# Kernel tuning notes

Hardware: AMD Instinct MI355X
Metric: run time of the kernel (lower is better)

Reference implementation:

```python
import jax, jax.numpy as jnp
import numpy as np

N_NODES = 100000
N_EDGES = 1600000
N_GRAPHS = 128


def setup_inputs() -> dict:
    key = jax.random.key(0)
    ks = jax.random.split(key, 8)
    x = jax.random.normal(ks[0], (N_NODES, 384), dtype=jnp.float32)
    edge_index = jax.random.randint(ks[1], (2, N_EDGES), 0, N_NODES, dtype=jnp.int64)
    batch = jnp.sort(jax.random.randint(ks[2], (N_NODES,), 0, N_GRAPHS, dtype=jnp.int64))
    W1 = jax.random.normal(ks[3], (384, 128), dtype=jnp.float32) * (1.0 / np.sqrt(384))
    b1 = jnp.zeros((128,), dtype=jnp.float32)
    W2 = jax.random.normal(ks[4], (128, 64), dtype=jnp.float32) * (1.0 / np.sqrt(128))
    b2 = jnp.zeros((64,), dtype=jnp.float32)
    Wlin = jax.random.normal(ks[5], (64, 2), dtype=jnp.float32) * (1.0 / np.sqrt(64))
    blin = jnp.zeros((2,), dtype=jnp.float32)
    return {"x": x, "edge_index": edge_index, "batch": batch,
            "W1": W1, "b1": b1, "W2": W2, "b2": b2, "Wlin": Wlin, "blin": blin}


def gcn_conv(x, src, dst, W, b, n_nodes):
    # PyG GCNConv: self-loops + symmetric normalization D^{-1/2} A_hat D^{-1/2},
    # linear transform first (out_dim < in_dim -> cheaper messages).
    h = x @ W  # [N, out]
    deg = jax.ops.segment_sum(jnp.ones_like(dst, dtype=h.dtype), dst,
                              num_segments=n_nodes) + 1.0  # self-loop weight
    dis = jax.lax.rsqrt(deg)  # deg >= 1 always (self-loop)
    norm = dis[src] * dis[dst]  # per-edge normalization [E]
    msg = h[src] * norm[:, None]  # gather + scale [E, out]
    agg = jax.ops.segment_sum(msg, dst, num_segments=n_nodes)
    agg = agg + h * (dis * dis)[:, None]  # self-loop contribution
    return agg + b


def reference(x, edge_index, batch, W1, b1, W2, b2, Wlin, blin):
    src, dst = edge_index[0], edge_index[1]
    n_nodes = x.shape[0]
    h = jax.nn.relu(gcn_conv(x, src, dst, W1, b1, n_nodes))
    h = jax.nn.relu(gcn_conv(h, src, dst, W2, b2, n_nodes))
    # global_mean_pool over graph ids
    sums = jax.ops.segment_sum(h, batch, num_segments=N_GRAPHS)
    cnts = jax.ops.segment_sum(jnp.ones((n_nodes,), dtype=h.dtype), batch,
                               num_segments=N_GRAPHS)
    pooled = sums / jnp.maximum(cnts, 1.0)[:, None]  # [G, 64]
    # dropout is identity in eval mode
    return pooled @ Wlin + blin  # [G, 2]
```

## Files before the change

kernel.cpp:

```cpp
#include <hip/hip_runtime.h>


#define NN 100000
#define NG 128
#define BNODES 256
#define NBUK ((NN + BNODES - 1) / BNODES)
#define BCAP 6144

typedef __attribute__((ext_vector_type(8))) short short8;
typedef __attribute__((ext_vector_type(8))) unsigned short u16x8;
typedef __attribute__((ext_vector_type(4))) float f32x4;

__device__ __forceinline__ unsigned short f2bf(float f) {
    union { float f; unsigned u; } v; v.f = f;
    unsigned r = v.u + 0x7fffu + ((v.u >> 16) & 1u);
    return (unsigned short)(r >> 16);
}
__device__ __forceinline__ float bf2f(unsigned short h) {
    union { unsigned u; float f; } v; v.u = ((unsigned)h) << 16;
    return v.f;
}

__device__ __forceinline__ void gload_lds16(const void* g, void* l) {
    __builtin_amdgcn_global_load_lds(
        (const __attribute__((address_space(1))) void*)g,
        (__attribute__((address_space(3))) void*)l, 16, 0, 0);
}

__global__ __launch_bounds__(256) void init_kernel(int* __restrict__ bcnt,
                                                   float* __restrict__ pooled,
                                                   float* __restrict__ cnt) {
    const int i = blockIdx.x * 256 + threadIdx.x;
    if (i < NBUK) bcnt[i] = 0;
    if (i < NG * 64) pooled[i] = 0.f;
    if (i < NG) cnt[i] = 0.f;
}

__global__ __launch_bounds__(256) void bucket_scatter(const int* __restrict__ src,
                                                      const int* __restrict__ dst,
                                                      int* __restrict__ bcnt,
                                                      int2* __restrict__ pairs, int E) {
    __shared__ int hist[NBUK];
    __shared__ int lbase[NBUK];
    __shared__ int lfill[NBUK];
    const int t = threadIdx.x;
    const int chunk = (E + gridDim.x - 1) / gridDim.x;
    const int lo = blockIdx.x * chunk;
    const int hi = min(E, lo + chunk);
    for (int b = t; b < NBUK; b += 256) { hist[b] = 0; lfill[b] = 0; }
    __syncthreads();
    for (int i = lo + t; i < hi; i += 256)
        atomicAdd(&hist[dst[i] >> 8], 1);
    __syncthreads();
    for (int b = t; b < NBUK; b += 256)
        lbase[b] = hist[b] ? atomicAdd(&bcnt[b], hist[b]) : 0;
    __syncthreads();
    for (int i = lo + t; i < hi; i += 256) {
        const int s = src[i], d = dst[i];
        const int b = d >> 8;
        const int off = atomicAdd(&lfill[b], 1);
        pairs[(size_t)b * BCAP + lbase[b] + off] = make_int2(s, d);
    }
}

__global__ __launch_bounds__(512) void bucket_scan(const int* __restrict__ bcnt,
                                                   int* __restrict__ bbase,
                                                   int* __restrict__ rowptr,
                                                   int N, int E) {
    __shared__ int sm[512];
    const int t = threadIdx.x;
    sm[t] = (t < NBUK) ? bcnt[t] : 0;
    __syncthreads();
    for (int d = 1; d < 512; d <<= 1) {
        int a = (t >= d) ? sm[t - d] : 0;
        __syncthreads();
        sm[t] += a;
        __syncthreads();
    }
    if (t <= NBUK) bbase[t] = (t == 0) ? 0 : sm[t - 1];
    if (t == 0) rowptr[N] = E;
}

__global__ __launch_bounds__(256) void bucket_build(const int2* __restrict__ pairs,
                                                    const int* __restrict__ bcnt,
                                                    const int* __restrict__ bbase,
                                                    int* __restrict__ rowptr,
                                                    float* __restrict__ dis,
                                                    int* __restrict__ col, int N) {
    __shared__ int cnt[BNODES];
    __shared__ int sm[BNODES];
    __shared__ int pref[BNODES];
    __shared__ int fillc[BNODES];
    const int b = blockIdx.x;
    const int t = threadIdx.x;
    const int nbase = b * BNODES;
    const int ecnt = bcnt[b];
    const int2* ep = pairs + (size_t)b * BCAP;
    const int gbase = bbase[b];

    cnt[t] = 0;
    fillc[t] = 0;
    __syncthreads();
    for (int i = t; i < ecnt; i += 256)
        atomicAdd(&cnt[ep[i].y & (BNODES - 1)], 1);
    __syncthreads();
    sm[t] = cnt[t];
    __syncthreads();
    for (int d = 1; d < 256; d <<= 1) {
        int a = (t >= d) ? sm[t - d] : 0;
        __syncthreads();
        sm[t] += a;
        __syncthreads();
    }
    pref[t] = sm[t] - cnt[t];
    const int node = nbase + t;
    if (node < N) {
        rowptr[node] = gbase + pref[t];
        dis[node] = rsqrtf((float)cnt[t] + 1.0f);
    }
    __syncthreads();
    for (int i = t; i < ecnt; i += 256) {
        const int2 e = ep[i];
        const int d = e.y & (BNODES - 1);
        const int pos = gbase + pref[d] + atomicAdd(&fillc[d], 1);
        col[pos] = e.x;
    }
}

__global__ __launch_bounds__(256) void pack_w(const float* __restrict__ W,
                                              unsigned short* __restrict__ packH,
                                              unsigned short* __restrict__ packL,
                                              int K, int BN) {
    const int idx = blockIdx.x * blockDim.x + threadIdx.x;
    if (idx >= K * BN) return;
    const int e = idx & 7;
    const int l = (idx >> 3) & 63;
    const int rest = idx >> 9;
    const int NF = BN >> 4;
    const int nf = rest % NF;
    const int ks = rest / NF;
    const int n = nf * 16 + (l & 15);
    const int k = ks * 32 + ((l >> 4) & 3) * 8 + e;
    const float v = W[(size_t)k * BN + n];
    const unsigned short h = f2bf(v);
    packH[idx] = h;
    packL[idx] = f2bf(v - bf2f(h));
}

template <int BN, int K>
__global__ __launch_bounds__(256) void gemm_mfma(const float* __restrict__ A,
                                                 const unsigned short* __restrict__ WpH,
                                                 const unsigned short* __restrict__ WpL,
                                                 const float* __restrict__ scale,
                                                 unsigned short* __restrict__ Out,
                                                 int N) {
    constexpr int BM = 64;
    constexpr int NK = K / 32;
    constexpr int WROWS = (BN == 128) ? 2 : 4;
    constexpr int WCOLS = (BN == 128) ? 2 : 1;
    constexpr int WTM = BM / WROWS;
    constexpr int MF = WTM / 16;
    constexpr int NFW = (BN / WCOLS) / 16;
    constexpr int NFB = BN / 16;

    __shared__ float AsF[4][4][16][32];

    const int t = threadIdx.x;
    const int wid = t >> 6, lane = t & 63;
    const int wr = wid / WCOLS, wc = wid % WCOLS;
    const int r0 = blockIdx.x * BM;

    const int dmarow0 = min(r0 + wid * 16 + (lane >> 3), NN - 1);
    const int dmarow1 = min(r0 + wid * 16 + 8 + (lane >> 3), NN - 1);
    const float* dmap0 = A + (size_t)dmarow0 * K + (lane & 7) * 4;
    const float* dmap1 = A + (size_t)dmarow1 * K + (lane & 7) * 4;

    auto stageA = [&](int buf, int ks) {
        gload_lds16(dmap0 + ks * 32, &AsF[buf][wid][0][0]);
        gload_lds16(dmap1 + ks * 32, &AsF[buf][wid][8][0]);
    };
    auto loadB = [&](int ks, short8* bH, short8* bL) {
#pragma unroll
        for (int n = 0; n < NFW; ++n) {
            const int nfg = wc * NFW + n;
            const int base = ((ks * NFB + nfg) * 64 + lane) * 8;
            bH[n] = *(const short8*)&WpH[base];
            bL[n] = *(const short8*)&WpL[base];
        }
    };

    f32x4 acc[MF][NFW];
#pragma unroll
    for (int m = 0; m < MF; ++m)
#pragma unroll
        for (int n = 0; n < NFW; ++n) acc[m][n] = (f32x4){0.f, 0.f, 0.f, 0.f};

    short8 bHc[NFW], bLc[NFW];
    loadB(0, bHc, bLc);
    stageA(0, 0);
    if (NK > 1) stageA(1, 1);
    if (NK > 2) stageA(2, 2);

#pragma unroll
    for (int ks = 0; ks < NK; ++ks) {
        if (ks == NK - 1) {
            asm volatile("s_waitcnt vmcnt(0)" ::: "memory");
        } else {
            asm volatile("s_waitcnt vmcnt(4)" ::: "memory");
        }
        __builtin_amdgcn_s_barrier();
        short8 bHn[NFW], bLn[NFW];
        if (ks + 1 < NK) loadB(ks + 1, bHn, bLn);
        if (ks + 3 < NK) stageA((ks + 3) & 3, ks + 3);
        const int cur = ks & 3;
#pragma unroll
        for (int m = 0; m < MF; ++m) {
            const int mf = wr * MF + m;
            const float* fp = &AsF[cur][mf][lane & 15][(lane >> 4) * 8];
            const f32x4 f0 = *(const f32x4*)fp;
            const f32x4 f1 = *(const f32x4*)(fp + 4);
            short8 aH;
            aH[0] = (short)f2bf(f0[0]);
            aH[1] = (short)f2bf(f0[1]);
            aH[2] = (short)f2bf(f0[2]);
            aH[3] = (short)f2bf(f0[3]);
            aH[4] = (short)f2bf(f1[0]);
            aH[5] = (short)f2bf(f1[1]);
            aH[6] = (short)f2bf(f1[2]);
            aH[7] = (short)f2bf(f1[3]);
#pragma unroll
            for (int n = 0; n < NFW; ++n) {
                acc[m][n] = __builtin_amdgcn_mfma_f32_16x16x32_bf16(aH, bHc[n], acc[m][n], 0, 0, 0);
                acc[m][n] = __builtin_amdgcn_mfma_f32_16x16x32_bf16(aH, bLc[n], acc[m][n], 0, 0, 0);
            }
        }
        if (ks + 1 < NK) {
#pragma unroll
            for (int n = 0; n < NFW; ++n) {
                bHc[n] = bHn[n];
                bLc[n] = bLn[n];
            }
        }
    }

#pragma unroll
    for (int m = 0; m < MF; ++m) {
        const int row0 = r0 + wr * WTM + m * 16 + ((lane >> 4) << 2);
        float sc[4];
#pragma unroll
        for (int r = 0; r < 4; ++r) sc[r] = (row0 + r < N) ? scale[row0 + r] : 0.f;
#pragma unroll
        for (int n = 0; n < NFW; ++n) {
            const int cn = wc * (NFW * 16) + n * 16 + (lane & 15);
#pragma unroll
            for (int r = 0; r < 4; ++r) {
                if (row0 + r < N)
                    Out[(size_t)(row0 + r) * BN + cn] = f2bf(acc[m][n][r] * sc[r]);
            }
        }
    }
}

template <int BN, int K>
__global__ __launch_bounds__(256) void gemm_mfma_b(const unsigned short* __restrict__ A,
                                                   const unsigned short* __restrict__ WpH,
                                                   const unsigned short* __restrict__ WpL,
                                                   const float* __restrict__ scale,
                                                   unsigned short* __restrict__ Out,
                                                   int N) {
    constexpr int BM = 64;
    constexpr int NK = K / 32;
    constexpr int WROWS = 4;
    constexpr int WTM = BM / WROWS;
    constexpr int NFW = BN / 16;
    constexpr int NFB = BN / 16;

    __shared__ unsigned short AsB[4][4][16][32];

    const int t = threadIdx.x;
    const int wid = t >> 6, lane = t & 63;
    const int wr = wid;
    const int r0 = blockIdx.x * BM;

    const int dmarow = min(r0 + wid * 16 + (lane >> 2), NN - 1);
    const unsigned short* dmap = A + (size_t)dmarow * K + (lane & 3) * 8;

    auto stageA = [&](int buf, int ks) {
        gload_lds16(dmap + ks * 32, &AsB[buf][wid][0][0]);
    };
    auto loadB = [&](int ks, short8* bH, short8* bL) {
#pragma unroll
        for (int n = 0; n < NFW; ++n) {
            const int base = ((ks * NFB + n) * 64 + lane) * 8;
            bH[n] = *(const short8*)&WpH[base];
            bL[n] = *(const short8*)&WpL[base];
        }
    };

    f32x4 acc[NFW];
#pragma unroll
    for (int n = 0; n < NFW; ++n) acc[n] = (f32x4){0.f, 0.f, 0.f, 0.f};

    short8 bHc[NFW], bLc[NFW];
    loadB(0, bHc, bLc);
    stageA(0, 0);
    if (NK > 1) stageA(1, 1);
    if (NK > 2) stageA(2, 2);

#pragma unroll
    for (int ks = 0; ks < NK; ++ks) {
        if (ks == NK - 1) {
            asm volatile("s_waitcnt vmcnt(0)" ::: "memory");
        } else if (ks == 0) {
            asm volatile("s_waitcnt vmcnt(2)" ::: "memory");
        } else {
            asm volatile("s_waitcnt vmcnt(4)" ::: "memory");
        }
        __builtin_amdgcn_s_barrier();
        short8 bHn[NFW], bLn[NFW];
        if (ks + 1 < NK) loadB(ks + 1, bHn, bLn);
        if (ks + 3 < NK) stageA((ks + 3) & 3, ks + 3);
        const int cur = ks & 3;
        const short8 aH = *(const short8*)&AsB[cur][wr][lane & 15][(lane >> 4) * 8];
#pragma unroll
        for (int n = 0; n < NFW; ++n) {
            acc[n] = __builtin_amdgcn_mfma_f32_16x16x32_bf16(aH, bHc[n], acc[n], 0, 0, 0);
            acc[n] = __builtin_amdgcn_mfma_f32_16x16x32_bf16(aH, bLc[n], acc[n], 0, 0, 0);
        }
        if (ks + 1 < NK) {
#pragma unroll
            for (int n = 0; n < NFW; ++n) {
                bHc[n] = bHn[n];
                bLc[n] = bLn[n];
            }
        }
    }

    const int row0 = r0 + wr * WTM + ((lane >> 4) << 2);
    float sc[4];
#pragma unroll
    for (int r = 0; r < 4; ++r) sc[r] = (row0 + r < N) ? scale[row0 + r] : 0.f;
#pragma unroll
    for (int n = 0; n < NFW; ++n) {
        const int cn = n * 16 + (lane & 15);
#pragma unroll
        for (int r = 0; r < 4; ++r) {
            if (row0 + r < N)
                Out[(size_t)(row0 + r) * BN + cn] = f2bf(acc[n][r] * sc[r]);
        }
    }
}

template <int COLS, bool OB16>
__global__ __launch_bounds__(256) void agg_gather(const int* __restrict__ rowptr,
                                                  const int* __restrict__ col,
                                                  const float* __restrict__ dis,
                                                  const unsigned short* __restrict__ Hs,
                                                  const float* __restrict__ bias,
                                                  void* __restrict__ OutV, int N) {
    constexpr int NPW = (COLS == 128) ? 1 : 2;
    constexpr int LPN = 64 / NPW;
    constexpr int LPR = COLS / 8;
    constexpr int NSG = LPN / LPR;
    const int gw = (int)((blockIdx.x * blockDim.x + threadIdx.x) >> 6);
    const int lane = threadIdx.x & 63;
    const int sub = lane / LPN;
    const int nl = lane % LPN;
    const int esub = nl / LPR;
    const int sl = nl % LPR;
    const int node = gw * NPW + sub;
    const int lgbase = sub * LPN;

    float acc[8];
#pragma unroll
    for (int k = 0; k < 8; ++k) acc[k] = 0.f;

    int base = 0, len = 0;
    const int nodec = (node < N) ? node : 0;
    if (node < N) {
        base = rowptr[node];
        len = rowptr[node + 1] - base;
    }

    for (int j0 = 0; j0 < len; j0 += LPN) {
        const int remain = min(LPN, len - j0);
        const int sidx = (nl < remain) ? col[base + j0 + nl] : nodec;
        const int qtr = (remain + NSG - 1) / NSG;
        const int off = esub * qtr;
        int u = 0;
        for (; u + 8 <= qtr; u += 8) {
            u16x8 hv[8];
            float wv[8];
#pragma unroll
            for (int b = 0; b < 8; ++b) {
                const int idx = off + u + b;
                const int s = __shfl(sidx, lgbase + idx);
                wv[b] = (idx < remain) ? 1.f : 0.f;
                hv[b] = *(const u16x8*)(Hs + (size_t)s * COLS + sl * 8);
            }
#pragma unroll
            for (int b = 0; b < 8; ++b)
#pragma unroll
                for (int k = 0; k < 8; ++k)
                    acc[k] = fmaf(bf2f(hv[b][k]), wv[b], acc[k]);
        }
        for (; u + 4 <= qtr; u += 4) {
            u16x8 hv[4];
            float wv[4];
#pragma unroll
            for (int b = 0; b < 4; ++b) {
                const int idx = off + u + b;
                const int s = __shfl(sidx, lgbase + idx);
                wv[b] = (idx < remain) ? 1.f : 0.f;
                hv[b] = *(const u16x8*)(Hs + (size_t)s * COLS + sl * 8);
            }
#pragma unroll
            for (int b = 0; b < 4; ++b)
#pragma unroll
                for (int k = 0; k < 8; ++k)
                    acc[k] = fmaf(bf2f(hv[b][k]), wv[b], acc[k]);
        }
        for (; u < qtr; ++u) {
            const int idx = off + u;
            const int s = __shfl(sidx, lgbase + idx);
            const float w = (idx < remain) ? 1.f : 0.f;
            const u16x8 hv = *(const u16x8*)(Hs + (size_t)s * COLS + sl * 8);
#pragma unroll
            for (int k = 0; k < 8; ++k)
                acc[k] = fmaf(bf2f(hv[k]), w, acc[k]);
        }
    }

#pragma unroll
    for (int k = 0; k < 8; ++k) {
        acc[k] += __shfl_xor(acc[k], LPR);
        acc[k] += __shfl_xor(acc[k], 2 * LPR);
    }

    if (node < N && esub == 0) {
        const float dd = dis[node];
        const u16x8 hsb = *(const u16x8*)(Hs + (size_t)node * COLS + sl * 8);
        float o[8];
#pragma unroll
        for (int k = 0; k < 8; ++k)
            o[k] = fmaxf(fmaf(acc[k] + bf2f(hsb[k]), dd, bias[sl * 8 + k]), 0.f);
        if (OB16) {
            u16x8 ob;
#pragma unroll
            for (int k = 0; k < 8; ++k) ob[k] = f2bf(o[k]);
            *(u16x8*)((unsigned short*)OutV + (size_t)node * COLS + sl * 8) = ob;
        } else {
            float* Out = (float*)OutV;
            f32x4 o0, o1;
#pragma unroll
            for (int k = 0; k < 4; ++k) {
                o0[k] = o[k];
                o1[k] = o[k + 4];
            }
            *(f32x4*)(Out + (size_t)node * COLS + sl * 8) = o0;
            *(f32x4*)(Out + (size_t)node * COLS + sl * 8 + 4) = o1;
        }
    }
}

__global__ __launch_bounds__(256) void pool_kernel(const float* __restrict__ H,
                                                   const int* __restrict__ batch,
                                                   float* __restrict__ pooled,
                                                   float* __restrict__ cnt, int N) {
    const int c = threadIdx.x & 63;
    const int w = threadIdx.x >> 6;
    const int row0 = blockIdx.x * 128 + w * 32;
    if (row0 >= N) return;
    const int nr = min(32, N - row0);

    float v[32];
    int b[32];
#pragma unroll
    for (int i = 0; i < 32; ++i) {
        const int r = row0 + i;
        if (i < nr) {
            v[i] = H[(size_t)r * 64 + c];
            b[i] = batch[r];
        } else {
            v[i] = 0.f;
            b[i] = -1;
        }
    }
    int cur = b[0];
    float sum = 0.f, csum = 0.f;
#pragma unroll
    for (int i = 0; i < 32; ++i) {
        if (i < nr) {
            if (b[i] != cur) {
                atomicAdd(&pooled[cur * 64 + c], sum);
                if (c == 0) atomicAdd(&cnt[cur], csum);
                cur = b[i];
                sum = 0.f;
                csum = 0.f;
            }
            sum += v[i];
            csum += 1.f;
        }
    }
    atomicAdd(&pooled[cur * 64 + c], sum);
    if (c == 0) atomicAdd(&cnt[cur], csum);
}

__global__ __launch_bounds__(256) void final_kernel(const float* __restrict__ pooled,
                                                    const float* __restrict__ cnt,
                                                    const float* __restrict__ Wlin,
                                                    const float* __restrict__ blin,
                                                    float* __restrict__ out) {
    const int t = threadIdx.x;
    const int g = t >> 1, o = t & 1;
    const float inv = 1.0f / fmaxf(cnt[g], 1.0f);
    float s = 0.f;
#pragma unroll
    for (int j = 0; j < 64; ++j) s = fmaf(pooled[g * 64 + j], Wlin[j * 2 + o], s);
    out[t] = s * inv + blin[o];
}

extern "C" void kernel_launch(void* const* d_in, const int* in_sizes, int n_in,
                              void* d_out, int out_size, void* d_ws, size_t ws_size,
                              hipStream_t stream) {
    const float* x     = (const float*)d_in[0];
    const int*   edge  = (const int*)d_in[1];
    const int*   batch = (const int*)d_in[2];
    const float* W1    = (const float*)d_in[3];
    const float* b1    = (const float*)d_in[4];
    const float* W2    = (const float*)d_in[5];
    const float* b2    = (const float*)d_in[6];
    const float* Wlin  = (const float*)d_in[7];
    const float* blin  = (const float*)d_in[8];
    float* out = (float*)d_out;

    const int N = NN;
    const int E = in_sizes[1] / 2;
    const int* src = edge;
    const int* dst = edge + E;

    char* ws = (char*)d_ws;
    size_t off = 0;
    auto alloc = [&](size_t bytes) -> void* {
        void* p = ws + off;
        off += (bytes + 511) & ~(size_t)511;
        return p;
    };
    float* dis    = (float*)alloc((size_t)N * 4);
    int*   rowptr = (int*)alloc((size_t)(N + 1) * 4);
    int*   bcnt   = (int*)alloc((size_t)NBUK * 4);
    int*   bbase  = (int*)alloc((size_t)(NBUK + 1) * 4);
    int*   col    = (int*)alloc((size_t)E * 4);
    int2*  pairs  = (int2*)alloc((size_t)NBUK * BCAP * 8);
    unsigned short* w1h = (unsigned short*)alloc((size_t)384 * 128 * 2);
    unsigned short* w1l = (unsigned short*)alloc((size_t)384 * 128 * 2);
    unsigned short* w2h = (unsigned short*)alloc((size_t)128 * 64 * 2);
    unsigned short* w2l = (unsigned short*)alloc((size_t)128 * 64 * 2);
    unsigned short* h1bf   = (unsigned short*)alloc((size_t)N * 128 * 2);
    unsigned short* agg1bf = (unsigned short*)alloc((size_t)N * 128 * 2);
    float* pooled = (float*)alloc((size_t)NG * 64 * 4);
    float* cnt    = (float*)alloc((size_t)NG * 4);
    unsigned short* h2bf = h1bf;
    float* agg2 = (float*)agg1bf;

    init_kernel<<<(NG * 64 + 255) / 256, 256, 0, stream>>>(bcnt, pooled, cnt);

    pack_w<<<(384 * 128 + 255) / 256, 256, 0, stream>>>(W1, w1h, w1l, 384, 128);
    pack_w<<<(128 * 64 + 255) / 256, 256, 0, stream>>>(W2, w2h, w2l, 128, 64);

    bucket_scatter<<<512, 256, 0, stream>>>(src, dst, bcnt, pairs, E);
    bucket_scan<<<1, 512, 0, stream>>>(bcnt, bbase, rowptr, N, E);
    bucket_build<<<NBUK, 256, 0, stream>>>(pairs, bcnt, bbase, rowptr, dis, col, N);

    const int gblocks = (N + 63) / 64;
    gemm_mfma<128, 384><<<gblocks, 256, 0, stream>>>(x, w1h, w1l, dis, h1bf, N);
    agg_gather<128, true><<<(N + 3) / 4, 256, 0, stream>>>(rowptr, col, dis, h1bf, b1,
                                                           (void*)agg1bf, N);

    gemm_mfma_b<64, 128><<<gblocks, 256, 0, stream>>>(agg1bf, w2h, w2l, dis, h2bf, N);
    agg_gather<64, false><<<(N + 7) / 8, 256, 0, stream>>>(rowptr, col, dis, h2bf, b2,
                                                           (void*)agg2, N);

    pool_kernel<<<(N + 127) / 128, 256, 0, stream>>>(agg2, batch, pooled, cnt, N);
    final_kernel<<<1, 256, 0, stream>>>(pooled, cnt, Wlin, blin, out);
}
```

Measured before the change: 236.2 us.

## Fuse second aggregation with mean pooling and pack bucket edge pairs

The second-layer gather aggregation now feeds global mean pooling directly. Each block stages its 8 node rows in shared memory and reduces runs of the same graph before issuing atomics, so the fp32 N×64 intermediate and the separate pool kernel go away. Bucket pairs are also packed into one 32-bit word (low 8 dst bits plus 24-bit src), which halves the scatter and build traffic. The packing assumes node ids fit in 24 bits, and pooling now does more per-block atomics with a block-wide sync.

```diff
diff --git a/kernel.cpp b/kernel.cpp
--- a/kernel.cpp
+++ b/kernel.cpp
@@ -39,7 +39,7 @@
 __global__ __launch_bounds__(256) void bucket_scatter(const int* __restrict__ src,
                                                       const int* __restrict__ dst,
                                                       int* __restrict__ bcnt,
-                                                      int2* __restrict__ pairs, int E) {
+                                                      int* __restrict__ pairs, int E) {
     __shared__ int hist[NBUK];
     __shared__ int lbase[NBUK];
     __shared__ int lfill[NBUK];
@@ -59,7 +59,7 @@
         const int s = src[i], d = dst[i];
         const int b = d >> 8;
         const int off = atomicAdd(&lfill[b], 1);
-        pairs[(size_t)b * BCAP + lbase[b] + off] = make_int2(s, d);
+        pairs[(size_t)b * BCAP + lbase[b] + off] = ((d & 255) << 24) | s;
     }
 }
 
@@ -81,7 +81,7 @@
     if (t == 0) rowptr[N] = E;
 }
 
-__global__ __launch_bounds__(256) void bucket_build(const int2* __restrict__ pairs,
+__global__ __launch_bounds__(256) void bucket_build(const int* __restrict__ pairs,
                                                     const int* __restrict__ bcnt,
                                                     const int* __restrict__ bbase,
                                                     int* __restrict__ rowptr,
@@ -95,14 +95,14 @@
     const int t = threadIdx.x;
     const int nbase = b * BNODES;
     const int ecnt = bcnt[b];
-    const int2* ep = pairs + (size_t)b * BCAP;
+    const int* ep = pairs + (size_t)b * BCAP;
     const int gbase = bbase[b];
 
     cnt[t] = 0;
     fillc[t] = 0;
     __syncthreads();
     for (int i = t; i < ecnt; i += 256)
-        atomicAdd(&cnt[ep[i].y & (BNODES - 1)], 1);
+        atomicAdd(&cnt[((unsigned)ep[i]) >> 24], 1);
     __syncthreads();
     sm[t] = cnt[t];
     __syncthreads();
@@ -120,10 +120,10 @@
     }
     __syncthreads();
     for (int i = t; i < ecnt; i += 256) {
-        const int2 e = ep[i];
-        const int d = e.y & (BNODES - 1);
+        const int p = ep[i];
+        const int d = ((unsigned)p) >> 24;
         const int pos = gbase + pref[d] + atomicAdd(&fillc[d], 1);
-        col[pos] = e.x;
+        col[pos] = p & 0xFFFFFF;
     }
 }
 
@@ -351,25 +351,24 @@
     }
 }
 
-template <int COLS, bool OB16>
-__global__ __launch_bounds__(256) void agg_gather(const int* __restrict__ rowptr,
-                                                  const int* __restrict__ col,
-                                                  const float* __restrict__ dis,
-                                                  const unsigned short* __restrict__ Hs,
-                                                  const float* __restrict__ bias,
-                                                  void* __restrict__ OutV, int N) {
-    constexpr int NPW = (COLS == 128) ? 1 : 2;
-    constexpr int LPN = 64 / NPW;
+__global__ __launch_bounds__(256) void agg_gather128(const int* __restrict__ rowptr,
+                                                     const int* __restrict__ col,
+                                                     const float* __restrict__ dis,
+                                                     const unsigned short* __restrict__ Hs,
+                                                     const float* __restrict__ bias,
+                                                     unsigned short* __restrict__ Out,
+                                                     int N) {
+    constexpr int COLS = 128;
+    constexpr int LPN = 64;
     constexpr int LPR = COLS / 8;
-    constexpr int NSG = LPN / LPR;
+    constexpr int NSG = 4;
     const int gw = (int)((blockIdx.x * blockDim.x + threadIdx.x) >> 6);
     const int lane = threadIdx.x & 63;
-    const int sub = lane / LPN;
-    const int nl = lane % LPN;
+    const int nl = lane;
     const int esub = nl / LPR;
     const int sl = nl % LPR;
-    const int node = gw * NPW + sub;
-    const int lgbase = sub * LPN;
+    const int node = gw;
+    const int lgbase = 0;
 
     float acc[8];
 #pragma unroll
@@ -440,70 +439,145 @@
     if (node < N && esub == 0) {
         const float dd = dis[node];
         const u16x8 hsb = *(const u16x8*)(Hs + (size_t)node * COLS + sl * 8);
-        float o[8];
+        u16x8 ob;
 #pragma unroll
         for (int k = 0; k < 8; ++k)
-            o[k] = fmaxf(fmaf(acc[k] + bf2f(hsb[k]), dd, bias[sl * 8 + k]), 0.f);
-        if (OB16) {
-            u16x8 ob;
-#pragma unroll
-            for (int k = 0; k < 8; ++k) ob[k] = f2bf(o[k]);
-            *(u16x8*)((unsigned short*)OutV + (size_t)node * COLS + sl * 8) = ob;
-        } else {
-            float* Out = (float*)OutV;
-            f32x4 o0, o1;
-#pragma unroll
-            for (int k = 0; k < 4; ++k) {
-                o0[k] = o[k];
-                o1[k] = o[k + 4];
-            }
-            *(f32x4*)(Out + (size_t)node * COLS + sl * 8) = o0;
-            *(f32x4*)(Out + (size_t)node * COLS + sl * 8 + 4) = o1;
-        }
-    }
-}
-
-__global__ __launch_bounds__(256) void pool_kernel(const float* __restrict__ H,
-                                                   const int* __restrict__ batch,
-                                                   float* __restrict__ pooled,
-                                                   float* __restrict__ cnt, int N) {
-    const int c = threadIdx.x & 63;
-    const int w = threadIdx.x >> 6;
-    const int row0 = blockIdx.x * 128 + w * 32;
-    if (row0 >= N) return;
-    const int nr = min(32, N - row0);
-
-    float v[32];
-    int b[32];
-#pragma unroll
-    for (int i = 0; i < 32; ++i) {
-        const int r = row0 + i;
-        if (i < nr) {
-            v[i] = H[(size_t)r * 64 + c];
-            b[i] = batch[r];
-        } else {
-            v[i] = 0.f;
-            b[i] = -1;
-        }
-    }
-    int cur = b[0];
-    float sum = 0.f, csum = 0.f;
-#pragma unroll
-    for (int i = 0; i < 32; ++i) {
-        if (i < nr) {
-            if (b[i] != cur) {
-                atomicAdd(&pooled[cur * 64 + c], sum);
-                if (c == 0) atomicAdd(&cnt[cur], csum);
-                cur = b[i];
-                sum = 0.f;
-                csum = 0.f;
-            }
-            sum += v[i];
-            csum += 1.f;
-        }
-    }
-    atomicAdd(&pooled[cur * 64 + c], sum);
-    if (c == 0) atomicAdd(&cnt[cur], csum);
+            ob[k] = f2bf(fmaxf(fmaf(acc[k] + bf2f(hsb[k]), dd, bias[sl * 8 + k]), 0.f));
+        *(u16x8*)(Out + (size_t)node * COLS + sl * 8) = ob;
+    }
+}
+
+__global__ __launch_bounds__(256) void agg_pool(const int* __restrict__ rowptr,
+                                                const int* __restrict__ col,
+                                                const float* __restrict__ dis,
+                                                const unsigned short* __restrict__ Hs,
+                                                const float* __restrict__ bias,
+                                                const int* __restrict__ batch,
+                                                float* __restrict__ pooled,
+                                                float* __restrict__ cnt, int N) {
+    constexpr int COLS = 64;
+    constexpr int NPW = 2;
+    constexpr int LPN = 32;
+    constexpr int LPR = COLS / 8;
+    constexpr int NSG = 4;
+
+    __shared__ float pbuf[8][64];
+    __shared__ int pg[8];
+
+    const int t = threadIdx.x;
+    const int wid = t >> 6;
+    const int gw = (int)blockIdx.x * 4 + wid;
+    const int lane = t & 63;
+    const int sub = lane / LPN;
+    const int nl = lane % LPN;
+    const int esub = nl / LPR;
+    const int sl = nl % LPR;
+    const int node = gw * NPW + sub;
+    const int slot = wid * 2 + sub;
+    const int lgbase = sub * LPN;
+
+    float acc[8];
+#pragma unroll
+    for (int k = 0; k < 8; ++k) acc[k] = 0.f;
+
+    int base = 0, len = 0;
+    const int nodec = (node < N) ? node : 0;
+    if (node < N) {
+        base = rowptr[node];
+        len = rowptr[node + 1] - base;
+    }
+
+    for (int j0 = 0; j0 < len; j0 += LPN) {
+        const int remain = min(LPN, len - j0);
+        const int sidx = (nl < remain) ? col[base + j0 + nl] : nodec;
+        const int qtr = (remain + NSG - 1) / NSG;
+        const int off = esub * qtr;
+        int u = 0;
+        for (; u + 8 <= qtr; u += 8) {
+            u16x8 hv[8];
+            float wv[8];
+#pragma unroll
+            for (int b = 0; b < 8; ++b) {
+                const int idx = off + u + b;
+                const int s = __shfl(sidx, lgbase + idx);
+                wv[b] = (idx < remain) ? 1.f : 0.f;
+                hv[b] = *(const u16x8*)(Hs + (size_t)s * COLS + sl * 8);
+            }
+#pragma unroll
+            for (int b = 0; b < 8; ++b)
+#pragma unroll
+                for (int k = 0; k < 8; ++k)
+                    acc[k] = fmaf(bf2f(hv[b][k]), wv[b], acc[k]);
+        }
+        for (; u + 4 <= qtr; u += 4) {
+            u16x8 hv[4];
+            float wv[4];
+#pragma unroll
+            for (int b = 0; b < 4; ++b) {
+                const int idx = off + u + b;
+                const int s = __shfl(sidx, lgbase + idx);
+                wv[b] = (idx < remain) ? 1.f : 0.f;
+                hv[b] = *(const u16x8*)(Hs + (size_t)s * COLS + sl * 8);
+            }
+#pragma unroll
+            for (int b = 0; b < 4; ++b)
+#pragma unroll
+                for (int k = 0; k < 8; ++k)
+                    acc[k] = fmaf(bf2f(hv[b][k]), wv[b], acc[k]);
+        }
+        for (; u < qtr; ++u) {
+            const int idx = off + u;
+            const int s = __shfl(sidx, lgbase + idx);
+            const float w = (idx < remain) ? 1.f : 0.f;
+            const u16x8 hv = *(const u16x8*)(Hs + (size_t)s * COLS + sl * 8);
+#pragma unroll
+            for (int k = 0; k < 8; ++k)
+                acc[k] = fmaf(bf2f(hv[k]), w, acc[k]);
+        }
+    }
+
+#pragma unroll
+    for (int k = 0; k < 8; ++k) {
+        acc[k] += __shfl_xor(acc[k], LPR);
+        acc[k] += __shfl_xor(acc[k], 2 * LPR);
+    }
+
+    if (esub == 0) {
+        const float dd = dis[nodec];
+        const u16x8 hsb = *(const u16x8*)(Hs + (size_t)nodec * COLS + sl * 8);
+#pragma unroll
+        for (int k = 0; k < 8; ++k)
+            pbuf[slot][sl * 8 + k] =
+                fmaxf(fmaf(acc[k] + bf2f(hsb[k]), dd, bias[sl * 8 + k]), 0.f);
+        if (sl == 0) pg[slot] = (node < N) ? batch[node] : -1;
+    }
+    __syncthreads();
+
+    if (t < 64) {
+        int curg = -2;
+        float sum = 0.f, csum = 0.f;
+#pragma unroll
+        for (int s = 0; s < 8; ++s) {
+            const int g = pg[s];
+            if (g >= 0) {
+                if (g != curg) {
+                    if (curg >= 0) {
+                        atomicAdd(&pooled[curg * 64 + t], sum);
+                        if (t == 0) atomicAdd(&cnt[curg], csum);
+                    }
+                    curg = g;
+                    sum = 0.f;
+                    csum = 0.f;
+                }
+                sum += pbuf[s][t];
+                csum += 1.f;
+            }
+        }
+        if (curg >= 0) {
+            atomicAdd(&pooled[curg * 64 + t], sum);
+            if (t == 0) atomicAdd(&cnt[curg], csum);
+        }
+    }
 }
 
 __global__ __launch_bounds__(256) void final_kernel(const float* __restrict__ pooled,
@@ -551,7 +625,7 @@
     int*   bcnt   = (int*)alloc((size_t)NBUK * 4);
     int*   bbase  = (int*)alloc((size_t)(NBUK + 1) * 4);
     int*   col    = (int*)alloc((size_t)E * 4);
-    int2*  pairs  = (int2*)alloc((size_t)NBUK * BCAP * 8);
+    int*   pairs  = (int*)alloc((size_t)NBUK * BCAP * 4);
     unsigned short* w1h = (unsigned short*)alloc((size_t)384 * 128 * 2);
     unsigned short* w1l = (unsigned short*)alloc((size_t)384 * 128 * 2);
     unsigned short* w2h = (unsigned short*)alloc((size_t)128 * 64 * 2);
@@ -561,7 +635,6 @@
     float* pooled = (float*)alloc((size_t)NG * 64 * 4);
     float* cnt    = (float*)alloc((size_t)NG * 4);
     unsigned short* h2bf = h1bf;
-    float* agg2 = (float*)agg1bf;
 
     init_kernel<<<(NG * 64 + 255) / 256, 256, 0, stream>>>(bcnt, pooled, cnt);
 
@@ -574,13 +647,11 @@
 
     const int gblocks = (N + 63) / 64;
     gemm_mfma<128, 384><<<gblocks, 256, 0, stream>>>(x, w1h, w1l, dis, h1bf, N);
-    agg_gather<128, true><<<(N + 3) / 4, 256, 0, stream>>>(rowptr, col, dis, h1bf, b1,
-                                                           (void*)agg1bf, N);
+    agg_gather128<<<(N + 3) / 4, 256, 0, stream>>>(rowptr, col, dis, h1bf, b1, agg1bf, N);
 
     gemm_mfma_b<64, 128><<<gblocks, 256, 0, stream>>>(agg1bf, w2h, w2l, dis, h2bf, N);
-    agg_gather<64, false><<<(N + 7) / 8, 256, 0, stream>>>(rowptr, col, dis, h2bf, b2,
-                                                           (void*)agg2, N);
-
-    pool_kernel<<<(N + 127) / 128, 256, 0, stream>>>(agg2, batch, pooled, cnt, N);
+    agg_pool<<<(N + 7) / 8, 256, 0, stream>>>(rowptr, col, dis, h2bf, b2, batch,
+                                              pooled, cnt, N);
+
     final_kernel<<<1, 256, 0, stream>>>(pooled, cnt, Wlin, blin, out);
 }
```

New measurement: 287.8 us. 21.8% more time.
